# Kernel optimization log

Measured on AMD Instinct MI355X. Metric: run time of the kernel, lower is better.

The kernel has to match this reference:

```python
import jax, jax.numpy as jnp
import numpy as np

V, D, DC, L, K, H, ND, S, B = 16, 256, 128, 3, 16, 4, 3, 900, 16
HD = D // H
DMETA = 17           # [confidence(1) | layer_id(8) | iter(4) | pass(4)]
DSLOT = DC + DMETA
MAX_ITERS, MAX_PASSES, WRITE_TOK = 2, 2, 64
FLOATS = ['token_embed','segment_embed','slot_embeddings','layer_id_embeddings',
          'Wq_read','Wk_read','Wv_read','Wg_read','bg_read','Wqkv','Wo',
          'Wwk','Wwv','Wwg','bwg','Wout','bout','prev_answer_embed','Wfb','bfb']


def setup_inputs():
    key = jax.random.key(0)
    ks = jax.random.split(key, 24)
    n = lambda i, shape: 0.02 * jax.random.normal(ks[i], shape, dtype=jnp.float32)
    return dict(
        demo_inputs=jax.random.randint(ks[0], (B, ND, S), 0, V),
        demo_outputs=jax.random.randint(ks[1], (B, ND, S), 0, V),
        test_input=jax.random.randint(ks[2], (B, S), 0, V),
        token_embed=n(3, (V, D)), segment_embed=n(4, (2, D)),
        slot_embeddings=n(5, (L, K, DC)), layer_id_embeddings=n(6, (L, 8)),
        Wq_read=n(7, (L, D, DC)), Wk_read=n(8, (L, DSLOT, DC)), Wv_read=n(9, (L, DSLOT, D)),
        Wg_read=n(10, (L, D, 1)), bg_read=jnp.zeros((L, 1)),
        Wqkv=n(11, (L, D, 3 * D)), Wo=n(12, (L, D, D)),
        Wwk=n(13, (L, D, DC)), Wwv=n(14, (L, D, DC)),
        Wwg=n(15, (L, 2 * DC, 1)), bwg=jnp.zeros((L, 1)),
        Wout=n(16, (D, V)), bout=jnp.zeros((V,)),
        prev_answer_embed=n(17, (V, D)),
        Wfb=n(18, (2 * D, D)), bfb=jnp.zeros((D,)),
    )


def make_rope(n, hd):
    inv = 1.0 / (10000.0 ** (jnp.arange(0, hd, 2, dtype=jnp.float32) / hd))
    f = jnp.arange(n, dtype=jnp.float32)[:, None] * inv[None, :]  # [N, hd/2]
    return jnp.cos(f), jnp.sin(f)


def apply_rope(x, cos, sin):  # x: [B,H,N,hd]
    x1, x2 = x[..., ::2], x[..., 1::2]
    r1 = x1 * cos - x2 * sin
    r2 = x1 * sin + x2 * cos
    return jnp.stack([r1, r2], axis=-1).reshape(x.shape)


def layer_step(h, cache, l, it, pas, cos, sin, p):
    Bsz, N, _ = h.shape
    s0 = l * K
    # --- read: cross-attention from sequence to full structured cache ---
    q = h @ p['Wq_read'][l]                                   # [B,N,DC]
    k = cache @ p['Wk_read'][l]                               # [B,LK,DC]
    v = cache @ p['Wv_read'][l]                               # [B,LK,D]
    attn = jax.nn.softmax(jnp.einsum('bnd,bmd->bnm', q, k) / np.float32(np.sqrt(DC)), axis=-1)
    read = jnp.einsum('bnm,bmd->bnd', attn, v)
    rgate = jax.nn.sigmoid(h @ p['Wg_read'][l] + p['bg_read'][l])
    h = h + rgate * read
    # --- linear self-attention with RoPE (use_linear_attention=True) ---
    qh, kh, vh = jnp.split(h @ p['Wqkv'][l], 3, axis=-1)
    heads = lambda x: x.reshape(Bsz, N, H, HD).transpose(0, 2, 1, 3)
    qh, kh, vh = heads(qh), heads(kh), heads(vh)
    qf = jax.nn.elu(apply_rope(qh, cos, sin)) + 1.0
    kf = jax.nn.elu(apply_rope(kh, cos, sin)) + 1.0
    kv = jnp.einsum('bhnd,bhne->bhde', kf, vh)                # [B,H,HD,HD]
    z = 1.0 / (jnp.einsum('bhnd,bhd->bhn', qf, kf.sum(axis=2)) + 1e-6)
    att = jnp.einsum('bhnd,bhde->bhne', qf, kv) * z[..., None]
    h = h + att.transpose(0, 2, 1, 3).reshape(Bsz, N, D) @ p['Wo'][l]
    # --- write: last max_write_tokens tokens -> this layer's slot block ---
    wt = h[:, -WRITE_TOK:]                                    # [B,64,D]
    wk, wv = wt @ p['Wwk'][l], wt @ p['Wwv'][l]               # [B,64,DC]
    sq = cache[:, s0:s0 + K, :DC]                             # slot content queries
    wattn = jax.nn.softmax(jnp.einsum('bkd,bmd->bkm', sq, wk) / np.float32(np.sqrt(DC)), axis=-1)
    new_c = jnp.einsum('bkm,bmd->bkd', wattn, wv)
    wgate = jax.nn.sigmoid(jnp.concatenate([sq, new_c], -1) @ p['Wwg'][l] + p['bwg'][l])
    it_oh = jax.nn.one_hot(min(it, 3), 4, dtype=h.dtype)
    ps_oh = jax.nn.one_hot(min(pas, 3), 4, dtype=h.dtype)
    cache = cache.at[:, s0:s0 + K, :DC].set(sq + wgate * new_c)
    cache = cache.at[:, s0:s0 + K, DC:DC + 1].set(wgate)      # confidence
    cache = cache.at[:, s0:s0 + K, DC + 9:DC + 13].set(jnp.broadcast_to(it_oh, (Bsz, K, 4)))
    cache = cache.at[:, s0:s0 + K, DC + 13:].set(jnp.broadcast_to(ps_oh, (Bsz, K, 4)))
    return h, cache


def _model(p, demo_inputs, demo_outputs, test_input):
    Bsz = test_input.shape[0]
    # interleave demo_in/demo_out pairs then append test input
    demos = jnp.stack([demo_inputs, demo_outputs], axis=2).reshape(Bsz, ND * 2 * S)
    full = jnp.concatenate([demos, test_input], axis=1)       # [B, 6300]
    N = full.shape[1]
    cur = p['token_embed'][full] + p['segment_embed'][0]      # [B,N,D]
    cos, sin = make_rope(N, HD)
    # initial cache: learned content | conf=0 | layer_id | iter=0 | pass=0
    content = jnp.broadcast_to(p['slot_embeddings'].reshape(L * K, DC), (Bsz, L * K, DC))
    lids = jnp.broadcast_to(p['layer_id_embeddings'][:, None, :], (L, K, 8)).reshape(L * K, 8)
    meta = jnp.concatenate([jnp.zeros((L * K, 1)), lids, jnp.zeros((L * K, 8))], axis=-1)
    cache = jnp.concatenate([content, jnp.broadcast_to(meta, (Bsz, L * K, DMETA))], axis=-1)
    ts = ND * 2 * S
    prev_logits = None
    for pas in range(MAX_PASSES):
        if pas > 0:  # answer feedback from previous pass predictions
            pae = p['prev_answer_embed'][jnp.argmax(prev_logits, axis=-1)]
            tr = cur[:, ts:ts + S]
            g = jax.nn.sigmoid(jnp.concatenate([tr, pae], -1) @ p['Wfb'] + p['bfb'])
            cur = cur.at[:, ts:ts + S].set(tr + g * pae)
        h = cur
        for l in range(L):
            for it in range(MAX_ITERS):
                h, cache = layer_step(h, cache, l, it, pas, cos, sin, p)
        prev_logits = h[:, ts:ts + S] @ p['Wout'] + p['bout']  # [B,S,V]
    return prev_logits


def reference(demo_inputs, demo_outputs, test_input, token_embed, segment_embed,
              slot_embeddings, layer_id_embeddings, Wq_read, Wk_read, Wv_read,
              Wg_read, bg_read, Wqkv, Wo, Wwk, Wwv, Wwg, bwg, Wout, bout,
              prev_answer_embed, Wfb, bfb):
    p = dict(zip(FLOATS, (token_embed, segment_embed, slot_embeddings, layer_id_embeddings,
                          Wq_read, Wk_read, Wv_read, Wg_read, bg_read, Wqkv, Wo,
                          Wwk, Wwv, Wwg, bwg, Wout, bout, prev_answer_embed, Wfb, bfb)))
    return _model(p, demo_inputs, demo_outputs, test_input)
```

## Files before the change

kernel.cpp:

```cpp
#include <hip/hip_runtime.h>
#include <math.h>

#define Bz 16
#define Sz 900
#define Vz 16
#define Dz 256
#define DCz 128
#define Hz 4
#define Nz 6300
#define TSz 5400
#define DSLOTz 145
#define NSLOTz 48
#define GXA 99

typedef unsigned short u16;
typedef unsigned int u32;

typedef __bf16 bf16x8 __attribute__((ext_vector_type(8)));
typedef float floatx4 __attribute__((ext_vector_type(4)));
union U8 { bf16x8 v; uint4 q; };

static __device__ __forceinline__ float sigm(float x){ return 1.0f/(1.0f+__expf(-x)); }
static __device__ __forceinline__ void fma4(float4& a, float s, float4 b){ a.x+=s*b.x; a.y+=s*b.y; a.z+=s*b.z; a.w+=s*b.w; }
static __device__ __forceinline__ float dot4(float4 a, float4 b){ return a.x*b.x + a.y*b.y + a.z*b.z + a.w*b.w; }
static __device__ __forceinline__ float4 f4z(){ float4 z; z.x=0.f; z.y=0.f; z.z=0.f; z.w=0.f; return z; }
static __device__ __forceinline__ float elu1(float x){ return x>0.f ? x+1.f : __expf(x); }
static __device__ __forceinline__ float fcomp(float4 v, int i){ return (i==0)?v.x:(i==1)?v.y:(i==2)?v.z:v.w; }

static __device__ __forceinline__ uint hi16(float x){
  uint u = __float_as_uint(x);
  return (u + 0x7fffu + ((u>>16)&1u)) >> 16;
}

typedef const void GV __attribute__((address_space(1)));
typedef void LV __attribute__((address_space(3)));
static __device__ __forceinline__ void gl16(const float* g, float* l){
  __builtin_amdgcn_global_load_lds((GV*)g, (LV*)l, 16, 0, 0);
}
static __device__ __forceinline__ void gl16b(const void* g, void* l){
  __builtin_amdgcn_global_load_lds((GV*)g, (LV*)l, 16, 0, 0);
}

__global__ void k_sentinel(float* out, int nelem){
  int i = blockIdx.x*256 + threadIdx.x;
  if (i < nelem) out[i] = 12345.0f;
}

__global__ void k_zero(float* p, int n){
  int i = blockIdx.x*256 + threadIdx.x;
  if (i < n) p[i] = 0.f;
}

__global__ void k_rope(float* cost, float* sint){
  int i = blockIdx.x*256 + threadIdx.x;
  if (i >= Nz*32) return;
  int n = i>>5, f = i&31;
  double invd = pow(10000.0, -(double)f/32.0);
  double fr = (double)n * invd;
  cost[i] = (float)cos(fr);
  sint[i] = (float)sin(fr);
}

__global__ void k_embed(const int* __restrict__ di, const int* __restrict__ dq,
                        const int* __restrict__ ti, const float* __restrict__ temb,
                        const float* __restrict__ semb, float* __restrict__ h){
  int i = blockIdx.x*256 + threadIdx.x;
  if (i >= Bz*Nz*64) return;
  int dv = i & 63; int bn = i >> 6; int n = bn % Nz; int b = bn / Nz;
  int tok;
  if (n < TSz){
    int nd = n/1800; int r = n - nd*1800;
    tok = (r < Sz) ? di[(b*3+nd)*Sz + r] : dq[(b*3+nd)*Sz + (r-Sz)];
  } else {
    tok = ti[b*Sz + (n-TSz)];
  }
  const float4* e4 = (const float4*)(temb + (size_t)tok*Dz);
  const float4* s4 = (const float4*)semb;
  float4 v = e4[dv]; float4 s = s4[dv];
  v.x += s.x; v.y += s.y; v.z += s.z; v.w += s.w;
  ((float4*)h)[(size_t)bn*64 + dv] = v;
}

__global__ void k_cache_init(const float* __restrict__ slot_emb, const float* __restrict__ lid,
                             float* __restrict__ cache){
  int i = blockIdx.x*256 + threadIdx.x;
  if (i >= Bz*NSLOTz*DSLOTz) return;
  int c = i % DSLOTz; int sc = (i / DSLOTz) % NSLOTz; int l = sc >> 4;
  float v = 0.f;
  if (c < DCz) v = slot_emb[sc*DCz + c];
  else if (c >= 129 && c < 137) v = lid[l*8 + (c-129)];
  cache[i] = v;
}

__global__ void k_pack_w(const float* __restrict__ Wqkv,
                         u16* __restrict__ wh, u16* __restrict__ wl){
  int i = blockIdx.x*256 + threadIdx.x;
  if (i >= 3*65536) return;
  int l = i >> 16; int r = i & 65535;
  int ks = r >> 13; int ct = (r>>9)&15; int lane = (r>>3)&63; int e = r&7;
  int k = ks*32 + ((lane>>4)<<3) + e;
  int c = ct*16 + (lane&15);
  float x = Wqkv[(size_t)l*196608 + (size_t)k*768 + c];
  uint hb = hi16(x);
  uint lb = hi16(x - __uint_as_float(hb<<16));
  wh[i] = (u16)hb; wl[i] = (u16)lb;
}

__global__ void k_pack_wkv(const float* __restrict__ Wqkv,
                           u16* __restrict__ wh, u16* __restrict__ wl){
  int i = blockIdx.x*256 + threadIdx.x;
  if (i >= 3*131072) return;
  int l = i / 131072; int r = i % 131072;
  int ks = r >> 14; int ct = (r>>9)&31; int lane = (r>>3)&63; int e = r&7;
  int k = ks*32 + ((lane>>4)<<3) + e;
  int c = ct*16 + (lane&15);
  float x = Wqkv[(size_t)l*196608 + (size_t)k*768 + 256 + c];
  uint hb = hi16(x);
  uint lb = hi16(x - __uint_as_float(hb<<16));
  wh[i] = (u16)hb; wl[i] = (u16)lb;
}

__global__ void k_pack_wr(const float* __restrict__ Wqr,
                          u16* __restrict__ wh, u16* __restrict__ wl){
  int i = blockIdx.x*256 + threadIdx.x;
  if (i >= 3*32768) return;
  int l = i >> 15; int r = i & 32767;
  int ks = r >> 12; int ct = (r>>9)&7; int lane = (r>>3)&63; int e = r&7;
  int k = ks*32 + ((lane>>4)<<3) + e;
  int c = ct*16 + (lane&15);
  float x = Wqr[(size_t)l*32768 + (size_t)k*DCz + c];
  uint hb = hi16(x);
  uint lb = hi16(x - __uint_as_float(hb<<16));
  wh[i] = (u16)hb; wl[i] = (u16)lb;
}

__global__ void k_pack_p(const float* __restrict__ pmat,
                         u16* __restrict__ ph, u16* __restrict__ pl){
  int i = blockIdx.x*256 + threadIdx.x;
  if (i >= 16*65536) return;
  int b = i >> 16; int r = i & 65535;
  int ks2 = r >> 13; int ct = (r>>9)&15; int lane = (r>>3)&63; int e = r&7;
  int c = ks2*32 + ((lane>>4)<<3) + e;
  int oc = ct*16 + (lane&15);
  float x = pmat[(((size_t)(b*4 + (c>>6)))*64 + (c&63))*256 + oc];
  uint hb = hi16(x);
  uint lb = hi16(x - __uint_as_float(hb<<16));
  ph[i] = (u16)hb; pl[i] = (u16)lb;
}

__global__ __launch_bounds__(384) void k_proj_cache(const float* __restrict__ cache,
    const float* __restrict__ Wk, const float* __restrict__ Wv,
    u16* __restrict__ krh, u16* __restrict__ krl,
    u16* __restrict__ vrh, u16* __restrict__ vrl){
  __shared__ float crow[DSLOTz];
  int b = blockIdx.x / NSLOTz, sc = blockIdx.x % NSLOTz;
  int t = threadIdx.x;
  const float* cp = cache + (size_t)(b*NSLOTz+sc)*DSLOTz;
  if (t < DSLOTz) crow[t] = cp[t];
  __syncthreads();
  if (t < DCz){
    float a = 0.f;
    for (int r2=0;r2<DSLOTz;r2++) a += crow[r2]*Wk[r2*DCz + t];
    uint hb = hi16(a);
    uint lb = hi16(a - __uint_as_float(hb<<16));
    int ks = t>>5, st = sc>>4, lane = (sc&15) | (((t>>3)&3)<<4), e = t&7;
    size_t idx = (size_t)b*6144 + (size_t)(((ks*3+st)*64 + lane)*8 + e);
    krh[idx] = (u16)hb; krl[idx] = (u16)lb;
  } else {
    int d = t - DCz;
    float a = 0.f;
    for (int r2=0;r2<DSLOTz;r2++) a += crow[r2]*Wv[r2*Dz + d];
    uint hb = hi16(a);
    uint lb = hi16(a - __uint_as_float(hb<<16));
    int ot = d>>4, ks2 = sc>>5, lane = (d&15) | (((sc>>3)&3)<<4), e = sc&7;
    size_t idx = (size_t)b*16384 + (size_t)(((ks2*16+ot)*64 + lane)*8 + e);
    vrh[idx] = (u16)hb; vrl[idx] = (u16)lb;
  }
}

#define RA2_BH 0
#define RA2_BL 5120
#define RA2_QBH 10240
#define RA2_QBL 30720
#define RA2_ABH 10240
#define RA2_ABL 20480
#define RA2_G  51200
#define RA2_WG 51456
__global__ __launch_bounds__(256) void k_read_attn(
    float* __restrict__ h,
    const u16* __restrict__ wqh, const u16* __restrict__ wql,
    const u16* __restrict__ krh, const u16* __restrict__ krl,
    const u16* __restrict__ vrh, const u16* __restrict__ vrl,
    const float* __restrict__ Wg, const float* __restrict__ bg){
  __shared__ float smem[13120];
  char* sb = (char*)smem;
  const int t = threadIdx.x;
  const int b = blockIdx.y;
  const int n0 = blockIdx.x*64;
  const int w = t>>6, lane = t&63, ln = t&15, lq = (t>>4)&3;
  float* hb = h + (size_t)b*Nz*Dz;
  ((float*)(sb+RA2_WG))[t] = Wg[t];
  floatx4 acc[2][4];
  #pragma unroll
  for (int i=0;i<2;i++)
    #pragma unroll
    for (int j=0;j<4;j++){ acc[i][j][0]=0.f; acc[i][j][1]=0.f; acc[i][j][2]=0.f; acc[i][j][3]=0.f; }
  for (int ks=0; ks<8; ks++){
    __syncthreads();
    {
      int n = n0 + (t>>2);
      const float* hp = hb + (size_t)n*Dz + ks*32 + (t&3)*8;
      float x[8];
      if (n < Nz){
        float4 v0 = *(const float4*)(hp);
        float4 v1 = *(const float4*)(hp+4);
        x[0]=v0.x; x[1]=v0.y; x[2]=v0.z; x[3]=v0.w;
        x[4]=v1.x; x[5]=v1.y; x[6]=v1.z; x[7]=v1.w;
      } else {
        #pragma unroll
        for (int e=0;e<8;e++) x[e]=0.f;
      }
      uint hw[4], lw[4];
      #pragma unroll
      for (int e=0;e<4;e++){
        uint h0=hi16(x[2*e]), h1=hi16(x[2*e+1]);
        uint l0=hi16(x[2*e]-__uint_as_float(h0<<16));
        uint l1=hi16(x[2*e+1]-__uint_as_float(h1<<16));
        hw[e]=h0|(h1<<16); lw[e]=l0|(l1<<16);
      }
      int a16 = (((t>>2)*5 + (t&3))<<4);
      *(uint4*)(sb + RA2_BH + a16) = make_uint4(hw[0],hw[1],hw[2],hw[3]);
      *(uint4*)(sb + RA2_BL + a16) = make_uint4(lw[0],lw[1],lw[2],lw[3]);
    }
    __syncthreads();
    U8 bh[4], bl[4];
    #pragma unroll
    for (int nt=0; nt<4; nt++){
      int a16 = (((nt*16+ln)*5 + lq)<<4);
      bh[nt].q = *(const uint4*)(sb + RA2_BH + a16);
      bl[nt].q = *(const uint4*)(sb + RA2_BL + a16);
    }
    #pragma unroll
    for (int mf=0; mf<2; mf++){
      U8 ah, al;
      size_t ai = ((size_t)(ks*8 + w*2 + mf))*512 + lane*8;
      ah.q = *(const uint4*)(wqh + ai);
      al.q = *(const uint4*)(wql + ai);
      #pragma unroll
      for (int nt=0; nt<4; nt++){
        acc[mf][nt] = __builtin_amdgcn_mfma_f32_16x16x32_bf16(ah.v, bh[nt].v, acc[mf][nt], 0,0,0);
        acc[mf][nt] = __builtin_amdgcn_mfma_f32_16x16x32_bf16(ah.v, bl[nt].v, acc[mf][nt], 0,0,0);
        acc[mf][nt] = __builtin_amdgcn_mfma_f32_16x16x32_bf16(al.v, bh[nt].v, acc[mf][nt], 0,0,0);
      }
    }
  }
  {
    int n = t>>2, kq = t&3;
    int nn = n0+n; int nc = (nn < Nz) ? nn : (Nz-1);
    const float* hp = hb + (size_t)nc*Dz + kq*64;
    const float* wgp = (const float*)(sb+RA2_WG) + kq*64;
    float a = 0.f;
    for (int k=0;k<64;k+=4){
      float4 hv = *(const float4*)(hp+k);
      float4 wv = *(const float4*)(wgp+k);
      a += dot4(hv,wv);
    }
    a += __shfl_xor(a,1,64);
    a += __shfl_xor(a,2,64);
    if (kq==0) ((float*)(sb+RA2_G))[n] = a;
  }
  {
    #pragma unroll
    for (int mf=0; mf<2; mf++){
      #pragma unroll
      for (int nt=0; nt<4; nt++){
        float v0 = acc[mf][nt][0], v1 = acc[mf][nt][1];
        float v2 = acc[mf][nt][2], v3 = acc[mf][nt][3];
        uint h0=hi16(v0), h1=hi16(v1), h2=hi16(v2), h3=hi16(v3);
        uint l0=hi16(v0-__uint_as_float(h0<<16));
        uint l1=hi16(v1-__uint_as_float(h1<<16));
        uint l2=hi16(v2-__uint_as_float(h2<<16));
        uint l3=hi16(v3-__uint_as_float(h3<<16));
        int a16 = (((nt*16+ln)*5 + (mf*2 + (lq>>1)))<<4) + ((lq&1)<<3);
        *(uint2*)(sb + RA2_QBH + w*5120 + a16) = make_uint2(h0|(h1<<16), h2|(h3<<16));
        *(uint2*)(sb + RA2_QBL + w*5120 + a16) = make_uint2(l0|(l1<<16), l2|(l3<<16));
      }
    }
  }
  __syncthreads();
  floatx4 sacc[3];
  #pragma unroll
  for (int st=0; st<3; st++){ sacc[st][0]=0.f; sacc[st][1]=0.f; sacc[st][2]=0.f; sacc[st][3]=0.f; }
  for (int ks=0; ks<4; ks++){
    U8 bh, bl;
    int a16 = (((w*16+ln)*5 + lq)<<4);
    bh.q = *(const uint4*)(sb + RA2_QBH + ks*5120 + a16);
    bl.q = *(const uint4*)(sb + RA2_QBL + ks*5120 + a16);
    #pragma unroll
    for (int st=0; st<3; st++){
      U8 ah, al;
      size_t ai = (size_t)b*6144 + ((size_t)(ks*3+st))*512 + lane*8;
      ah.q = *(const uint4*)(krh + ai);
      al.q = *(const uint4*)(krl + ai);
      sacc[st] = __builtin_amdgcn_mfma_f32_16x16x32_bf16(ah.v, bh.v, sacc[st], 0,0,0);
      sacc[st] = __builtin_amdgcn_mfma_f32_16x16x32_bf16(ah.v, bl.v, sacc[st], 0,0,0);
      sacc[st] = __builtin_amdgcn_mfma_f32_16x16x32_bf16(al.v, bh.v, sacc[st], 0,0,0);
    }
  }
  {
    const float scl = 0.088388347648318447f;
    float mx = -1e30f;
    #pragma unroll
    for (int st=0; st<3; st++)
      #pragma unroll
      for (int r=0;r<4;r++){ sacc[st][r] *= scl; mx = fmaxf(mx, sacc[st][r]); }
    mx = fmaxf(mx, __shfl_xor(mx, 16, 64));
    mx = fmaxf(mx, __shfl_xor(mx, 32, 64));
    float su = 0.f;
    #pragma unroll
    for (int st=0; st<3; st++)
      #pragma unroll
      for (int r=0;r<4;r++){ float e = __expf(sacc[st][r]-mx); sacc[st][r]=e; su+=e; }
    su += __shfl_xor(su, 16, 64);
    su += __shfl_xor(su, 32, 64);
    float inv = 1.f/su;
    #pragma unroll
    for (int st=0; st<3; st++)
      #pragma unroll
      for (int r=0;r<4;r++) sacc[st][r] *= inv;
  }
  __syncthreads();
  {
    uint2 ah2[3], al2[3];
    #pragma unroll
    for (int st=0; st<3; st++){
      float v0=sacc[st][0], v1=sacc[st][1], v2=sacc[st][2], v3=sacc[st][3];
      uint h0=hi16(v0), h1=hi16(v1), h2=hi16(v2), h3=hi16(v3);
      uint l0=hi16(v0-__uint_as_float(h0<<16));
      uint l1=hi16(v1-__uint_as_float(h1<<16));
      uint l2=hi16(v2-__uint_as_float(h2<<16));
      uint l3=hi16(v3-__uint_as_float(h3<<16));
      ah2[st] = make_uint2(h0|(h1<<16), h2|(h3<<16));
      al2[st] = make_uint2(l0|(l1<<16), l2|(l3<<16));
    }
    int rb = (w*16+ln)*5;
    int sub = (lq&1)<<3;
    #pragma unroll
    for (int st=0; st<2; st++){
      int a16 = ((rb + st*2 + (lq>>1))<<4) + sub;
      *(uint2*)(sb + RA2_ABH + a16) = ah2[st];
      *(uint2*)(sb + RA2_ABL + a16) = al2[st];
    }
    {
      int a16 = ((rb + (lq>>1))<<4) + sub;
      *(uint2*)(sb + RA2_ABH + 5120 + a16) = ah2[2];
      *(uint2*)(sb + RA2_ABL + 5120 + a16) = al2[2];
      int z16 = ((rb + 2 + (lq>>1))<<4) + sub;
      *(uint2*)(sb + RA2_ABH + 5120 + z16) = make_uint2(0,0);
      *(uint2*)(sb + RA2_ABL + 5120 + z16) = make_uint2(0,0);
    }
  }
  __syncthreads();
  floatx4 o[4][4];
  #pragma unroll
  for (int i=0;i<4;i++)
    #pragma unroll
    for (int j=0;j<4;j++){ o[i][j][0]=0.f; o[i][j][1]=0.f; o[i][j][2]=0.f; o[i][j][3]=0.f; }
  #pragma unroll
  for (int ks2=0; ks2<2; ks2++){
    U8 bh[4], bl[4];
    #pragma unroll
    for (int nt=0; nt<4; nt++){
      int a16 = (((nt*16+ln)*5 + lq)<<4);
      bh[nt].q = *(const uint4*)(sb + RA2_ABH + ks2*5120 + a16);
      bl[nt].q = *(const uint4*)(sb + RA2_ABL + ks2*5120 + a16);
    }
    #pragma unroll
    for (int mf=0; mf<4; mf++){
      U8 ah, al;
      size_t ai = (size_t)b*16384 + ((size_t)(ks2*16 + w*4 + mf))*512 + lane*8;
      ah.q = *(const uint4*)(vrh + ai);
      al.q = *(const uint4*)(vrl + ai);
      #pragma unroll
      for (int nt=0; nt<4; nt++){
        o[mf][nt] = __builtin_amdgcn_mfma_f32_16x16x32_bf16(ah.v, bh[nt].v, o[mf][nt], 0,0,0);
        o[mf][nt] = __builtin_amdgcn_mfma_f32_16x16x32_bf16(ah.v, bl[nt].v, o[mf][nt], 0,0,0);
        o[mf][nt] = __builtin_amdgcn_mfma_f32_16x16x32_bf16(al.v, bh[nt].v, o[mf][nt], 0,0,0);
      }
    }
  }
  float bg0 = bg[0];
  #pragma unroll
  for (int nt=0; nt<4; nt++){
    int n = n0 + nt*16 + ln;
    if (n < Nz){
      float gv = sigm(((const float*)(sb+RA2_G))[nt*16+ln] + bg0);
      #pragma unroll
      for (int mf=0; mf<4; mf++){
        float* hp = hb + (size_t)n*Dz + w*64 + mf*16 + lq*4;
        float4 hv = *(const float4*)hp;
        hv.x += gv*o[mf][nt][0];
        hv.y += gv*o[mf][nt][1];
        hv.z += gv*o[mf][nt][2];
        hv.w += gv*o[mf][nt][3];
        *(float4*)hp = hv;
      }
    }
  }
}

#define KV_AH 0
#define KV_AL 16384
#define KV_BH 32768
#define KV_BL 37888
__global__ __launch_bounds__(256) void k_kv(
    const float* __restrict__ h,
    const u16* __restrict__ wh, const u16* __restrict__ wl,
    const float* __restrict__ cost, const float* __restrict__ sint,
    float* __restrict__ kvbuf){
  __shared__ float smem[10752];
  char* sb = (char*)smem;
  const int t = threadIdx.x;
  const int b = blockIdx.y;
  const int n0 = blockIdx.x*64;
  const int w = t>>6;
  const int lane = t&63;
  const int ln = t&15;
  const int lq = (t>>4)&3;
  const float* hb = h + (size_t)b*Nz*Dz;
  floatx4 acc[2][4][4];
  #pragma unroll
  for (int cp=0;cp<2;cp++)
    #pragma unroll
    for (int i=0;i<4;i++)
      #pragma unroll
      for (int j=0;j<4;j++){ acc[cp][i][j][0]=0.f; acc[cp][i][j][1]=0.f; acc[cp][i][j][2]=0.f; acc[cp][i][j][3]=0.f; }

  for (int ks=0; ks<8; ks++){
    __syncthreads();
    #pragma unroll
    for (int j=0;j<4;j++){
      int ct = w*4 + j;
      gl16b(wh + (((size_t)ks*32 + ct)<<9) + lane*8, sb + KV_AH + ct*1024);
      gl16b(wl + (((size_t)ks*32 + ct)<<9) + lane*8, sb + KV_AL + ct*1024);
    }
    {
      int n = n0 + (t>>2);
      const float* hp = hb + (size_t)n*Dz + ks*32 + (t&3)*8;
      float x[8];
      if (n < Nz){
        float4 v0 = *(const float4*)(hp);
        float4 v1 = *(const float4*)(hp+4);
        x[0]=v0.x; x[1]=v0.y; x[2]=v0.z; x[3]=v0.w;
        x[4]=v1.x; x[5]=v1.y; x[6]=v1.z; x[7]=v1.w;
      } else {
        #pragma unroll
        for (int e=0;e<8;e++) x[e]=0.f;
      }
      uint hw[4], lw[4];
      #pragma unroll
      for (int e=0;e<4;e++){
        uint h0=hi16(x[2*e]), h1=hi16(x[2*e+1]);
        uint l0=hi16(x[2*e]-__uint_as_float(h0<<16));
        uint l1=hi16(x[2*e+1]-__uint_as_float(h1<<16));
        hw[e]=h0|(h1<<16); lw[e]=l0|(l1<<16);
      }
      int a16 = (((t>>2)*5 + (t&3))<<4);
      *(uint4*)(sb + KV_BH + a16) = make_uint4(hw[0],hw[1],hw[2],hw[3]);
      *(uint4*)(sb + KV_BL + a16) = make_uint4(lw[0],lw[1],lw[2],lw[3]);
    }
    __syncthreads();
    U8 bh[4], bl[4];
    #pragma unroll
    for (int nt=0; nt<4; nt++){
      int a16 = (((nt*16+ln)*5 + lq)<<4);
      bh[nt].q = *(const uint4*)(sb + KV_BH + a16);
      bl[nt].q = *(const uint4*)(sb + KV_BL + a16);
    }
    #pragma unroll
    for (int mf=0; mf<4; mf++){
      U8 ah, al;
      int a16 = (((w*4+mf)*64 + lane)<<4);
      ah.q = *(const uint4*)(sb + KV_AH + a16);
      al.q = *(const uint4*)(sb + KV_AL + a16);
      #pragma unroll
      for (int nt=0; nt<4; nt++){
        acc[0][mf][nt] = __builtin_amdgcn_mfma_f32_16x16x32_bf16(ah.v, bh[nt].v, acc[0][mf][nt], 0,0,0);
        acc[0][mf][nt] = __builtin_amdgcn_mfma_f32_16x16x32_bf16(ah.v, bl[nt].v, acc[0][mf][nt], 0,0,0);
        acc[0][mf][nt] = __builtin_amdgcn_mfma_f32_16x16x32_bf16(al.v, bh[nt].v, acc[0][mf][nt], 0,0,0);
      }
    }
    __syncthreads();
    #pragma unroll
    for (int j=0;j<4;j++){
      int tl = w*4 + j;
      int ct = 16 + tl;
      gl16b(wh + (((size_t)ks*32 + ct)<<9) + lane*8, sb + KV_AH + tl*1024);
      gl16b(wl + (((size_t)ks*32 + ct)<<9) + lane*8, sb + KV_AL + tl*1024);
    }
    __syncthreads();
    #pragma unroll
    for (int mf=0; mf<4; mf++){
      U8 ah, al;
      int a16 = (((w*4+mf)*64 + lane)<<4);
      ah.q = *(const uint4*)(sb + KV_AH + a16);
      al.q = *(const uint4*)(sb + KV_AL + a16);
      #pragma unroll
      for (int nt=0; nt<4; nt++){
        acc[1][mf][nt] = __builtin_amdgcn_mfma_f32_16x16x32_bf16(ah.v, bh[nt].v, acc[1][mf][nt], 0,0,0);
        acc[1][mf][nt] = __builtin_amdgcn_mfma_f32_16x16x32_bf16(ah.v, bl[nt].v, acc[1][mf][nt], 0,0,0);
        acc[1][mf][nt] = __builtin_amdgcn_mfma_f32_16x16x32_bf16(al.v, bh[nt].v, acc[1][mf][nt], 0,0,0);
      }
    }
  }
  #pragma unroll
  for (int mf=0; mf<4; mf++){
    #pragma unroll
    for (int nt=0; nt<4; nt++){
      int n = n0 + nt*16 + ln;
      int valid = (n < Nz);
      int nc = valid ? n : (Nz-1);
      int pi = mf*8 + lq*2;
      float2 c2 = *(const float2*)(cost + (size_t)nc*32 + pi);
      float2 s2 = *(const float2*)(sint + (size_t)nc*32 + pi);
      float q0 = acc[0][mf][nt][0], q1 = acc[0][mf][nt][1];
      float q2 = acc[0][mf][nt][2], q3 = acc[0][mf][nt][3];
      float r0 = elu1(q0*c2.x - q1*s2.x);
      float r1 = elu1(q0*s2.x + q1*c2.x);
      float r2 = elu1(q2*c2.y - q3*s2.y);
      float r3 = elu1(q2*s2.y + q3*c2.y);
      acc[0][mf][nt][0] = valid ? r0 : 0.f;
      acc[0][mf][nt][1] = valid ? r1 : 0.f;
      acc[0][mf][nt][2] = valid ? r2 : 0.f;
      acc[0][mf][nt][3] = valid ? r3 : 0.f;
    }
  }
  const int d = t&63, q4 = t>>6;
  float* kvb = kvbuf + (size_t)(b*Hz)*4160;
  float* kfL = smem;
  float* vL  = smem + 4352;
  for (int g=0; g<4; g++){
    __syncthreads();
    if (w == g){
      #pragma unroll
      for (int mf=0; mf<4; mf++){
        #pragma unroll
        for (int nt=0; nt<4; nt++){
          int n = nt*16 + ln;
          int cc = mf*16 + lq*4;
          *(float4*)(kfL + n*68 + cc) = make_float4(acc[0][mf][nt][0],acc[0][mf][nt][1],acc[0][mf][nt][2],acc[0][mf][nt][3]);
          *(float4*)(vL  + n*68 + cc) = make_float4(acc[1][mf][nt][0],acc[1][mf][nt][1],acc[1][mf][nt][2],acc[1][mf][nt][3]);
        }
      }
    }
    __syncthreads();
    float4 kvacc[4];
    #pragma unroll
    for (int u=0;u<4;u++) kvacc[u]=f4z();
    float ksl = 0.f;
    for (int row=0; row<64; row++){
      float kd = kfL[row*68 + d];
      ksl += kd;
      const float4* vp = (const float4*)(vL + row*68);
      #pragma unroll
      for (int u=0;u<4;u++) fma4(kvacc[u], kd, vp[q4*4+u]);
    }
    float* kq = kvb + g*4160;
    #pragma unroll
    for (int u=0;u<4;u++){
      int e = q4*16 + 4*u;
      atomicAdd(&kq[(e+0)*64+d], kvacc[u].x);
      atomicAdd(&kq[(e+1)*64+d], kvacc[u].y);
      atomicAdd(&kq[(e+2)*64+d], kvacc[u].z);
      atomicAdd(&kq[(e+3)*64+d], kvacc[u].w);
    }
    if (q4==0) atomicAdd(&kq[4096+d], ksl);
  }
}

__global__ __launch_bounds__(256) void k_pmat(const float* __restrict__ kvbuf,
    const float* __restrict__ Wo, float* __restrict__ pmat){
  __shared__ float smem[8448];
  const int t = threadIdx.x;
  const int bh = blockIdx.x;
  const int hh = bh & 3;
  const int c0 = t&15, rr = t>>4;
  const float* kvp = kvbuf + (size_t)bh*4160;
  for (int id=t; id<4096; id+=256){
    int e=id>>6, d=id&63;
    smem[e*68+d] = kvp[id];
  }
  float4 acc[4][4];
  #pragma unroll
  for (int i=0;i<4;i++){
    #pragma unroll
    for (int j=0;j<4;j++) acc[i][j]=f4z();
  }
  for (int kt=0; kt<64; kt+=16){
    __syncthreads();
    for (int id=t; id<1024; id+=256){
      int wr=id>>6, cf=id&63;
      ((float4*)(smem+4352))[wr*64+cf] = ((const float4*)(Wo + (size_t)(hh*64+kt+wr)*256))[cf];
    }
    __syncthreads();
    for (int kk=0; kk<16; kk++){
      float4 a4 = *(const float4*)(smem + (kt+kk)*68 + 4*rr);
      const float4* wrow = (const float4*)(smem+4352) + kk*64;
      float4 w0=wrow[c0], w1=wrow[c0+16], w2=wrow[c0+32], w3=wrow[c0+48];
      #pragma unroll
      for (int i=0;i<4;i++){
        float ac = fcomp(a4,i);
        fma4(acc[i][0],ac,w0); fma4(acc[i][1],ac,w1); fma4(acc[i][2],ac,w2); fma4(acc[i][3],ac,w3);
      }
    }
  }
  float* Pp = pmat + (size_t)bh*16384;
  #pragma unroll
  for (int i=0;i<4;i++){
    #pragma unroll
    for (int j=0;j<4;j++) ((float4*)Pp)[(4*rr+i)*64 + c0 + 16*j] = acc[i][j];
  }
}

#define AH_OFF 0
#define AL_OFF 16384
#define BH_OFF 32768
#define BL_OFF 37888
#define KS_OFF 43008
__global__ __launch_bounds__(256) void k_att(
    float* __restrict__ h,
    const u16* __restrict__ wqh, const u16* __restrict__ wql,
    const u16* __restrict__ pth, const u16* __restrict__ ptl,
    const float* __restrict__ kvbuf,
    const float* __restrict__ cost, const float* __restrict__ sint){
  __shared__ float smem[11008];
  char* sb = (char*)smem;
  const int t = threadIdx.x;
  const int b = blockIdx.y;
  const int n0 = blockIdx.x*64;
  const int w = t>>6;
  const int lane = t&63;
  const int ln = t&15;
  const int lq = (t>>4)&3;
  float* hb = h + (size_t)b*Nz*Dz;
  ((float*)(sb+KS_OFF))[t] = kvbuf[(size_t)(b*Hz + w)*4160 + 4096 + lane];
  floatx4 acc[4][4];
  #pragma unroll
  for (int i=0;i<4;i++)
    #pragma unroll
    for (int j=0;j<4;j++){ acc[i][j][0]=0.f; acc[i][j][1]=0.f; acc[i][j][2]=0.f; acc[i][j][3]=0.f; }

  for (int ks=0; ks<8; ks++){
    __syncthreads();
    const u16* sh = wqh + (size_t)ks*8192;
    const u16* sl = wql + (size_t)ks*8192;
    #pragma unroll
    for (int j=0;j<4;j++){
      int c = w*4 + j;
      gl16b(sh + c*512 + lane*8, sb + AH_OFF + c*1024);
      gl16b(sl + c*512 + lane*8, sb + AL_OFF + c*1024);
    }
    {
      int n = n0 + (t>>2);
      const float* hp = hb + (size_t)n*Dz + ks*32 + (t&3)*8;
      float x[8];
      if (n < Nz){
        float4 v0 = *(const float4*)(hp);
        float4 v1 = *(const float4*)(hp+4);
        x[0]=v0.x; x[1]=v0.y; x[2]=v0.z; x[3]=v0.w;
        x[4]=v1.x; x[5]=v1.y; x[6]=v1.z; x[7]=v1.w;
      } else {
        #pragma unroll
        for (int e=0;e<8;e++) x[e]=0.f;
      }
      uint hw[4], lw[4];
      #pragma unroll
      for (int e=0;e<4;e++){
        uint h0=hi16(x[2*e]), h1=hi16(x[2*e+1]);
        uint l0=hi16(x[2*e]-__uint_as_float(h0<<16));
        uint l1=hi16(x[2*e+1]-__uint_as_float(h1<<16));
        hw[e]=h0|(h1<<16); lw[e]=l0|(l1<<16);
      }
      int a16 = (((t>>2)*5 + (t&3))<<4);
      *(uint4*)(sb + BH_OFF + a16) = make_uint4(hw[0],hw[1],hw[2],hw[3]);
      *(uint4*)(sb + BL_OFF + a16) = make_uint4(lw[0],lw[1],lw[2],lw[3]);
    }
    __syncthreads();
    U8 bh[4], bl[4];
    #pragma unroll
    for (int nt=0; nt<4; nt++){
      int a16 = (((nt*16+ln)*5 + lq)<<4);
      bh[nt].q = *(const uint4*)(sb + BH_OFF + a16);
      bl[nt].q = *(const uint4*)(sb + BL_OFF + a16);
    }
    #pragma unroll
    for (int mf=0; mf<4; mf++){
      U8 ah, al;
      int a16 = (((w*4+mf)*64 + lane)<<4);
      ah.q = *(const uint4*)(sb + AH_OFF + a16);
      al.q = *(const uint4*)(sb + AL_OFF + a16);
      #pragma unroll
      for (int nt=0; nt<4; nt++){
        acc[mf][nt] = __builtin_amdgcn_mfma_f32_16x16x32_bf16(ah.v, bh[nt].v, acc[mf][nt], 0,0,0);
        acc[mf][nt] = __builtin_amdgcn_mfma_f32_16x16x32_bf16(ah.v, bl[nt].v, acc[mf][nt], 0,0,0);
        acc[mf][nt] = __builtin_amdgcn_mfma_f32_16x16x32_bf16(al.v, bh[nt].v, acc[mf][nt], 0,0,0);
      }
    }
  }
  uint2 qzh[4][4], qzl[4][4];
  {
    float4 ks4[4];
    #pragma unroll
    for (int mf=0; mf<4; mf++)
      ks4[mf] = *(const float4*)(sb + KS_OFF + ((w*64 + mf*16 + lq*4)<<2));
    float psum[4] = {0.f,0.f,0.f,0.f};
    #pragma unroll
    for (int mf=0; mf<4; mf++){
      #pragma unroll
      for (int nt=0; nt<4; nt++){
        int n = n0 + nt*16 + ln;
        int nc = (n < Nz) ? n : (Nz-1);
        int pi = mf*8 + lq*2;
        float2 c2 = *(const float2*)(cost + (size_t)nc*32 + pi);
        float2 s2 = *(const float2*)(sint + (size_t)nc*32 + pi);
        float q0 = acc[mf][nt][0], q1 = acc[mf][nt][1];
        float q2 = acc[mf][nt][2], q3 = acc[mf][nt][3];
        float r0 = elu1(q0*c2.x - q1*s2.x);
        float r1 = elu1(q0*s2.x + q1*c2.x);
        float r2 = elu1(q2*c2.y - q3*s2.y);
        float r3 = elu1(q2*s2.y + q3*c2.y);
        acc[mf][nt][0]=r0; acc[mf][nt][1]=r1; acc[mf][nt][2]=r2; acc[mf][nt][3]=r3;
        psum[nt] += r0*ks4[mf].x + r1*ks4[mf].y + r2*ks4[mf].z + r3*ks4[mf].w;
      }
    }
    float zt[4];
    #pragma unroll
    for (int nt=0; nt<4; nt++){
      float p = psum[nt];
      p += __shfl_xor(p, 16, 64);
      p += __shfl_xor(p, 32, 64);
      zt[nt] = 1.f/(p + 1e-6f);
    }
    #pragma unroll
    for (int mf=0; mf<4; mf++){
      #pragma unroll
      for (int nt=0; nt<4; nt++){
        float v0 = acc[mf][nt][0]*zt[nt];
        float v1 = acc[mf][nt][1]*zt[nt];
        float v2 = acc[mf][nt][2]*zt[nt];
        float v3 = acc[mf][nt][3]*zt[nt];
        uint h0=hi16(v0), h1=hi16(v1), h2=hi16(v2), h3=hi16(v3);
        qzh[mf][nt] = make_uint2(h0|(h1<<16), h2|(h3<<16));
        uint l0=hi16(v0-__uint_as_float(h0<<16));
        uint l1=hi16(v1-__uint_as_float(h1<<16));
        uint l2=hi16(v2-__uint_as_float(h2<<16));
        uint l3=hi16(v3-__uint_as_float(h3<<16));
        qzl[mf][nt] = make_uint2(l0|(l1<<16), l2|(l3<<16));
      }
    }
  }
  floatx4 acc2[4][4];
  #pragma unroll
  for (int i=0;i<4;i++)
    #pragma unroll
    for (int j=0;j<4;j++){ acc2[i][j][0]=0.f; acc2[i][j][1]=0.f; acc2[i][j][2]=0.f; acc2[i][j][3]=0.f; }
  for (int ks2=0; ks2<8; ks2++){
    __syncthreads();
    const u16* sh = pth + (size_t)(b*8 + ks2)*8192;
    const u16* sl = ptl + (size_t)(b*8 + ks2)*8192;
    #pragma unroll
    for (int j=0;j<4;j++){
      int c = w*4 + j;
      gl16b(sh + c*512 + lane*8, sb + AH_OFF + c*1024);
      gl16b(sl + c*512 + lane*8, sb + AL_OFF + c*1024);
    }
    if (w == (ks2>>1)){
      #pragma unroll
      for (int mm=0; mm<2; mm++){
        int mf = ((ks2&1)<<1) + mm;
        int g = (mm<<1) + (lq>>1);
        int sub = (lq&1)*8;
        #pragma unroll
        for (int nt=0; nt<4; nt++){
          int a16 = (((nt*16+ln)*5 + g)<<4) + sub;
          *(uint2*)(sb + BH_OFF + a16) = qzh[mf][nt];
          *(uint2*)(sb + BL_OFF + a16) = qzl[mf][nt];
        }
      }
    }
    __syncthreads();
    U8 bh[4], bl[4];
    #pragma unroll
    for (int nt=0; nt<4; nt++){
      int a16 = (((nt*16+ln)*5 + lq)<<4);
      bh[nt].q = *(const uint4*)(sb + BH_OFF + a16);
      bl[nt].q = *(const uint4*)(sb + BL_OFF + a16);
    }
    #pragma unroll
    for (int mf=0; mf<4; mf++){
      U8 ah, al;
      int a16 = (((w*4+mf)*64 + lane)<<4);
      ah.q = *(const uint4*)(sb + AH_OFF + a16);
      al.q = *(const uint4*)(sb + AL_OFF + a16);
      #pragma unroll
      for (int nt=0; nt<4; nt++){
        acc2[mf][nt] = __builtin_amdgcn_mfma_f32_16x16x32_bf16(ah.v, bh[nt].v, acc2[mf][nt], 0,0,0);
        acc2[mf][nt] = __builtin_amdgcn_mfma_f32_16x16x32_bf16(ah.v, bl[nt].v, acc2[mf][nt], 0,0,0);
        acc2[mf][nt] = __builtin_amdgcn_mfma_f32_16x16x32_bf16(al.v, bh[nt].v, acc2[mf][nt], 0,0,0);
      }
    }
  }
  #pragma unroll
  for (int mf=0; mf<4; mf++){
    #pragma unroll
    for (int nt=0; nt<4; nt++){
      int n = n0 + nt*16 + ln;
      if (n < Nz){
        float* hp = hb + (size_t)n*Dz + w*64 + mf*16 + lq*4;
        float4 hv = *(const float4*)hp;
        hv.x += acc2[mf][nt][0];
        hv.y += acc2[mf][nt][1];
        hv.z += acc2[mf][nt][2];
        hv.w += acc2[mf][nt][3];
        *(float4*)hp = hv;
      }
    }
  }
}

__global__ __launch_bounds__(256) void k_wkv(const float* __restrict__ h,
    const float* __restrict__ Wwk, const float* __restrict__ Wwv,
    float* __restrict__ wkbuf, float* __restrict__ wvbuf){
  __shared__ float wtL[16*257];
  int t = threadIdx.x;
  int b = blockIdx.y, m0 = blockIdx.x*16;
  const float* hb = h + ((size_t)b*Nz + (Nz-64))*Dz;
  for (int i=t;i<16*Dz;i+=256){ int r=i>>8,c=i&255; wtL[r*257+c] = hb[(size_t)(m0+r)*Dz + c]; }
  __syncthreads();
  int r=t>>4, c0=t&15;
  float4 ak0=f4z(),ak1=f4z(),av0=f4z(),av1=f4z();
  for (int kk=0;kk<Dz;kk++){
    float hv = wtL[r*257+kk];
    const float4* wk4 = (const float4*)(Wwk + (size_t)kk*DCz);
    const float4* wv4 = (const float4*)(Wwv + (size_t)kk*DCz);
    fma4(ak0,hv,wk4[c0]); fma4(ak1,hv,wk4[c0+16]);
    fma4(av0,hv,wv4[c0]); fma4(av1,hv,wv4[c0+16]);
  }
  float4* ok = (float4*)(wkbuf + (size_t)(b*64 + m0+r)*DCz);
  float4* ov = (float4*)(wvbuf + (size_t)(b*64 + m0+r)*DCz);
  ok[c0]=ak0; ok[c0+16]=ak1; ov[c0]=av0; ov[c0+16]=av1;
}

__global__ __launch_bounds__(256) void k_cache_upd(float* __restrict__ cache,
    const float* __restrict__ wkbuf, const float* __restrict__ wvbuf,
    const float* __restrict__ Wwg, const float* __restrict__ bwg,
    int s0, int it, int pas){
  __shared__ float sqL[16*132];
  __shared__ float wkL[64*132];
  __shared__ float wat[16*68];
  __shared__ float ncL[16*132];
  __shared__ float wg[16];
  int t = threadIdx.x; int b = blockIdx.x;
  for (int i=t;i<16*DCz;i+=256){ int k2=i>>7,c=i&127; sqL[k2*132+c] = cache[((size_t)(b*NSLOTz)+s0+k2)*DSLOTz + c]; }
  for (int i=t;i<64*DCz;i+=256){ int m=i>>7,c=i&127; wkL[m*132+c] = wkbuf[(size_t)(b*64+m)*DCz+c]; }
  __syncthreads();
  {
    int k2 = t>>4;
    const float4* s4 = (const float4*)(sqL) + k2*33;
    for (int mm=0;mm<4;mm++){
      int m = (t&15) + 16*mm;
      const float4* k4 = (const float4*)(wkL) + m*33;
      float a=0.f;
      for (int d4=0;d4<32;d4++) a += dot4(s4[d4], k4[d4]);
      wat[k2*68+m] = a * 0.088388347648318447f;
    }
  }
  __syncthreads();
  if (t<16){
    float mx=-1e30f;
    for (int m=0;m<64;m++) mx = fmaxf(mx, wat[t*68+m]);
    float su=0.f;
    for (int m=0;m<64;m++){ float e=__expf(wat[t*68+m]-mx); wat[t*68+m]=e; su+=e; }
    float inv=1.f/su;
    for (int m=0;m<64;m++) wat[t*68+m]*=inv;
  }
  __syncthreads();
  {
    int k2=t>>4, c0=t&15;
    float4 a0=f4z(), a1=f4z();
    const float4* wvg = (const float4*)(wvbuf + (size_t)b*64*DCz);
    for (int m=0;m<64;m++){
      float a = wat[k2*68+m];
      fma4(a0,a,wvg[m*32+c0]); fma4(a1,a,wvg[m*32+c0+16]);
    }
    ((float4*)ncL)[k2*33+c0]=a0; ((float4*)ncL)[k2*33+16+c0]=a1;
  }
  __syncthreads();
  if (t<16){
    float a = bwg[0];
    for (int d2=0; d2<DCz; d2++) a += sqL[t*132+d2]*Wwg[d2] + ncL[t*132+d2]*Wwg[DCz+d2];
    wg[t] = sigm(a);
  }
  __syncthreads();
  for (int i=t;i<16*DCz;i+=256){
    int k2=i>>7,c=i&127;
    cache[((size_t)(b*NSLOTz)+s0+k2)*DSLOTz + c] = sqL[k2*132+c] + wg[k2]*ncL[k2*132+c];
  }
  if (t<16){
    float* cp = cache + ((size_t)(b*NSLOTz)+s0+t)*DSLOTz;
    cp[128] = wg[t];
    cp[137] = (it==0)?1.f:0.f; cp[138] = (it==1)?1.f:0.f; cp[139]=0.f; cp[140]=0.f;
    cp[141] = (pas==0)?1.f:0.f; cp[142] = (pas==1)?1.f:0.f; cp[143]=0.f; cp[144]=0.f;
  }
}

__global__ __launch_bounds__(256) void k_logits(const float* __restrict__ h,
    const float* __restrict__ Wout, const float* __restrict__ bout, float* __restrict__ out){
  __shared__ float hl[16*257];
  int t = threadIdx.x; int row0 = blockIdx.x*16;
  for (int i=t;i<16*Dz;i+=256){
    int rr=i>>8,c=i&255; int row=row0+rr; int b=row/Sz, s=row-b*Sz;
    hl[rr*257+c] = h[((size_t)b*Nz + TSz + s)*Dz + c];
  }
  __syncthreads();
  int rr = t>>4, v = t&15;
  float a = bout[v];
  for (int c=0;c<Dz;c++) a += hl[rr*257+c]*Wout[c*Vz + v];
  out[(size_t)(row0+rr)*Vz + v] = a;
}

__global__ __launch_bounds__(256) void k_feedback(float* __restrict__ h,
    const float* __restrict__ logits0, const float* __restrict__ pae,
    const float* __restrict__ Wfb, const float* __restrict__ bfb){
  __shared__ float trL[16*257];
  __shared__ float paeL[16*257];
  __shared__ int amL[16];
  int t = threadIdx.x; int b = blockIdx.y; int s0 = blockIdx.x*16;
  if (t<16){
    int s = s0+t; int am=0;
    if (s < Sz){
      const float* lg = logits0 + (size_t)(b*Sz+s)*Vz;
      float best = lg[0];
      for (int v=1;v<16;v++){ if (lg[v] > best){ best=lg[v]; am=v; } }
    }
    amL[t]=am;
  }
  for (int i=t;i<16*Dz;i+=256){
    int rr=i>>8,c=i&255; int s=s0+rr;
    trL[rr*257+c] = (s<Sz)? h[((size_t)b*Nz + TSz + s)*Dz + c] : 0.f;
  }
  __syncthreads();
  for (int i=t;i<16*Dz;i+=256){ int rr=i>>8,c=i&255; paeL[rr*257+c] = pae[(size_t)amL[rr]*Dz + c]; }
  __syncthreads();
  int r=t>>4, c0=t&15;
  float4 acc[4]; acc[0]=f4z(); acc[1]=f4z(); acc[2]=f4z(); acc[3]=f4z();
  for (int kk=0;kk<Dz;kk++){
    float xv = trL[r*257+kk];
    const float4* wr = (const float4*)(Wfb + (size_t)kk*Dz);
    fma4(acc[0],xv,wr[c0]); fma4(acc[1],xv,wr[c0+16]); fma4(acc[2],xv,wr[c0+32]); fma4(acc[3],xv,wr[c0+48]);
  }
  for (int kk=0;kk<Dz;kk++){
    float xv = paeL[r*257+kk];
    const float4* wr = (const float4*)(Wfb + (size_t)(Dz+kk)*Dz);
    fma4(acc[0],xv,wr[c0]); fma4(acc[1],xv,wr[c0+16]); fma4(acc[2],xv,wr[c0+32]); fma4(acc[3],xv,wr[c0+48]);
  }
  int s = s0+r;
  if (s < Sz){
    float* cp = h + ((size_t)b*Nz + TSz + s)*Dz;
    #pragma unroll
    for (int j=0;j<4;j++){
      float vals[4] = {acc[j].x, acc[j].y, acc[j].z, acc[j].w};
      #pragma unroll
      for (int q2=0;q2<4;q2++){
        int c = (c0+16*j)*4 + q2;
        float g = sigm(vals[q2] + bfb[c]);
        cp[c] = trL[r*257+c] + g*paeL[r*257+c];
      }
    }
  }
}

extern "C" void kernel_launch(void* const* d_in, const int* in_sizes, int n_in,
                              void* d_out, int out_size, void* d_ws, size_t ws_size,
                              hipStream_t stream){
  (void)in_sizes; (void)n_in;
  const int*   demo_in   = (const int*)d_in[0];
  const int*   demo_out  = (const int*)d_in[1];
  const int*   test_in   = (const int*)d_in[2];
  const float* token_emb = (const float*)d_in[3];
  const float* seg_emb   = (const float*)d_in[4];
  const float* slot_emb  = (const float*)d_in[5];
  const float* lid_emb   = (const float*)d_in[6];
  const float* Wq_read   = (const float*)d_in[7];
  const float* Wk_read   = (const float*)d_in[8];
  const float* Wv_read   = (const float*)d_in[9];
  const float* Wg_read   = (const float*)d_in[10];
  const float* bg_read   = (const float*)d_in[11];
  const float* Wqkv      = (const float*)d_in[12];
  const float* Wo        = (const float*)d_in[13];
  const float* Wwk       = (const float*)d_in[14];
  const float* Wwv       = (const float*)d_in[15];
  const float* Wwg       = (const float*)d_in[16];
  const float* bwg       = (const float*)d_in[17];
  const float* Wout      = (const float*)d_in[18];
  const float* bout      = (const float*)d_in[19];
  const float* pae       = (const float*)d_in[20];
  const float* Wfb       = (const float*)d_in[21];
  const float* bfb       = (const float*)d_in[22];

  char* wsb = (char*)d_ws;
  size_t off = 0;
  auto alloc = [&](size_t bytes)->char*{
    char* p = wsb + off;
    off += (bytes + 255) & ~(size_t)255;
    return p;
  };
  float* hbuf   = (float*)alloc((size_t)Bz*Nz*Dz*4);
  float* cache  = (float*)alloc((size_t)Bz*NSLOTz*DSLOTz*4);
  float* kvbuf  = (float*)alloc((size_t)Bz*Hz*4160*4);
  float* pmat   = (float*)alloc((size_t)Bz*Hz*64*256*4);
  float* wkbuf  = (float*)alloc((size_t)Bz*64*DCz*4);
  float* wvbuf  = (float*)alloc((size_t)Bz*64*DCz*4);
  float* logits0= (float*)alloc((size_t)Bz*Sz*Vz*4);
  float* cost   = (float*)alloc((size_t)Nz*32*4);
  float* sint   = (float*)alloc((size_t)Nz*32*4);
  u16*   wqth   = (u16*)alloc((size_t)3*65536*2);
  u16*   wqtl   = (u16*)alloc((size_t)3*65536*2);
  u16*   pth    = (u16*)alloc((size_t)16*65536*2);
  u16*   ptl    = (u16*)alloc((size_t)16*65536*2);
  u16*   wkvh   = (u16*)alloc((size_t)3*131072*2);
  u16*   wkvl   = (u16*)alloc((size_t)3*131072*2);
  u16*   wqrh   = (u16*)alloc((size_t)3*32768*2);
  u16*   wqrl   = (u16*)alloc((size_t)3*32768*2);
  u16*   krh    = (u16*)alloc((size_t)Bz*6144*2);
  u16*   krl    = (u16*)alloc((size_t)Bz*6144*2);
  u16*   vrh    = (u16*)alloc((size_t)Bz*16384*2);
  u16*   vrl    = (u16*)alloc((size_t)Bz*16384*2);

  if (off > ws_size){
    k_sentinel<<<(out_size+255)/256, 256, 0, stream>>>((float*)d_out, out_size);
    return;
  }

  k_rope<<<(Nz*32+255)/256, 256, 0, stream>>>(cost, sint);
  k_cache_init<<<(Bz*NSLOTz*DSLOTz+255)/256, 256, 0, stream>>>(slot_emb, lid_emb, cache);
  k_pack_w<<<768, 256, 0, stream>>>(Wqkv, wqth, wqtl);
  k_pack_wkv<<<1536, 256, 0, stream>>>(Wqkv, wkvh, wkvl);
  k_pack_wr<<<384, 256, 0, stream>>>(Wq_read, wqrh, wqrl);
  k_zero<<<512, 256, 0, stream>>>((float*)vrh, Bz*16384/2);
  k_zero<<<512, 256, 0, stream>>>((float*)vrl, Bz*16384/2);

  const int KVN = Bz*Hz*4160;
  for (int pas=0; pas<2; pas++){
    k_embed<<<(Bz*Nz*64+255)/256, 256, 0, stream>>>(demo_in, demo_out, test_in, token_emb, seg_emb, hbuf);
    if (pas==1)
      k_feedback<<<dim3(57,Bz), 256, 0, stream>>>(hbuf, logits0, pae, Wfb, bfb);
    for (int l=0; l<3; l++){
      for (int it=0; it<2; it++){
        k_proj_cache<<<Bz*NSLOTz, 384, 0, stream>>>(cache,
            Wk_read + (size_t)l*DSLOTz*DCz, Wv_read + (size_t)l*DSLOTz*Dz,
            krh, krl, vrh, vrl);
        k_read_attn<<<dim3(GXA,Bz), 256, 0, stream>>>(hbuf,
            wqrh + (size_t)l*32768, wqrl + (size_t)l*32768,
            krh, krl, vrh, vrl,
            Wg_read + (size_t)l*Dz, bg_read + l);
        k_zero<<<(KVN+255)/256, 256, 0, stream>>>(kvbuf, KVN);
        k_kv<<<dim3(GXA,Bz), 256, 0, stream>>>(hbuf,
            wkvh + (size_t)l*131072, wkvl + (size_t)l*131072, cost, sint, kvbuf);
        k_pmat<<<Bz*Hz, 256, 0, stream>>>(kvbuf, Wo + (size_t)l*Dz*Dz, pmat);
        k_pack_p<<<4096, 256, 0, stream>>>(pmat, pth, ptl);
        k_att<<<dim3(GXA,Bz), 256, 0, stream>>>(hbuf,
            wqth + (size_t)l*65536, wqtl + (size_t)l*65536, pth, ptl,
            kvbuf, cost, sint);
        k_wkv<<<dim3(4,Bz), 256, 0, stream>>>(hbuf,
            Wwk + (size_t)l*Dz*DCz, Wwv + (size_t)l*Dz*DCz, wkbuf, wvbuf);
        k_cache_upd<<<Bz, 256, 0, stream>>>(cache, wkbuf, wvbuf,
            Wwg + (size_t)l*2*DCz, bwg + l, l*16, it, pas);
      }
    }
    float* outp = (pas==0) ? logits0 : (float*)d_out;
    k_logits<<<900, 256, 0, stream>>>(hbuf, Wout, bout, outp);
  }
}
```

Measured before the change: 8.263 ms.

## Replace k_kv atomics with per-block partials and load weights directly from global

k_kv now reads the packed Wkv fragments straight from global memory into registers instead of staging them through shared memory, which removes several barriers per k-step and shrinks LDS use. When workspace allows, each block writes its KV partial sums to a dedicated buffer instead of using atomicAdd, and k_pmat reduces the 99 partials serially. The zeroing kernel is skipped in that mode. The cost is a large extra workspace buffer and a serial 99-way reduction inside only 64 k_pmat blocks, which could become a bottleneck.

New measurement: 9.425 ms. 1.14x slower.

```diff
diff --git a/kernel.cpp b/kernel.cpp
--- a/kernel.cpp
+++ b/kernel.cpp
@@ -409,16 +409,14 @@
   }
 }
 
-#define KV_AH 0
-#define KV_AL 16384
-#define KV_BH 32768
-#define KV_BL 37888
+#define KV_BH 0
+#define KV_BL 5120
 __global__ __launch_bounds__(256) void k_kv(
     const float* __restrict__ h,
     const u16* __restrict__ wh, const u16* __restrict__ wl,
     const float* __restrict__ cost, const float* __restrict__ sint,
-    float* __restrict__ kvbuf){
-  __shared__ float smem[10752];
+    float* __restrict__ kvpart, float* __restrict__ kvbuf, int use_part){
+  __shared__ float smem[8704];
   char* sb = (char*)smem;
   const int t = threadIdx.x;
   const int b = blockIdx.y;
@@ -438,12 +436,6 @@
 
   for (int ks=0; ks<8; ks++){
     __syncthreads();
-    #pragma unroll
-    for (int j=0;j<4;j++){
-      int ct = w*4 + j;
-      gl16b(wh + (((size_t)ks*32 + ct)<<9) + lane*8, sb + KV_AH + ct*1024);
-      gl16b(wl + (((size_t)ks*32 + ct)<<9) + lane*8, sb + KV_AL + ct*1024);
-    }
     {
       int n = n0 + (t>>2);
       const float* hp = hb + (size_t)n*Dz + ks*32 + (t&3)*8;
@@ -478,38 +470,19 @@
       bl[nt].q = *(const uint4*)(sb + KV_BL + a16);
     }
     #pragma unroll
-    for (int mf=0; mf<4; mf++){
-      U8 ah, al;
-      int a16 = (((w*4+mf)*64 + lane)<<4);
-      ah.q = *(const uint4*)(sb + KV_AH + a16);
-      al.q = *(const uint4*)(sb + KV_AL + a16);
-      #pragma unroll
-      for (int nt=0; nt<4; nt++){
-        acc[0][mf][nt] = __builtin_amdgcn_mfma_f32_16x16x32_bf16(ah.v, bh[nt].v, acc[0][mf][nt], 0,0,0);
-        acc[0][mf][nt] = __builtin_amdgcn_mfma_f32_16x16x32_bf16(ah.v, bl[nt].v, acc[0][mf][nt], 0,0,0);
-        acc[0][mf][nt] = __builtin_amdgcn_mfma_f32_16x16x32_bf16(al.v, bh[nt].v, acc[0][mf][nt], 0,0,0);
-      }
-    }
-    __syncthreads();
-    #pragma unroll
-    for (int j=0;j<4;j++){
-      int tl = w*4 + j;
-      int ct = 16 + tl;
-      gl16b(wh + (((size_t)ks*32 + ct)<<9) + lane*8, sb + KV_AH + tl*1024);
-      gl16b(wl + (((size_t)ks*32 + ct)<<9) + lane*8, sb + KV_AL + tl*1024);
-    }
-    __syncthreads();
-    #pragma unroll
-    for (int mf=0; mf<4; mf++){
-      U8 ah, al;
-      int a16 = (((w*4+mf)*64 + lane)<<4);
-      ah.q = *(const uint4*)(sb + KV_AH + a16);
-      al.q = *(const uint4*)(sb + KV_AL + a16);
-      #pragma unroll
-      for (int nt=0; nt<4; nt++){
-        acc[1][mf][nt] = __builtin_amdgcn_mfma_f32_16x16x32_bf16(ah.v, bh[nt].v, acc[1][mf][nt], 0,0,0);
-        acc[1][mf][nt] = __builtin_amdgcn_mfma_f32_16x16x32_bf16(ah.v, bl[nt].v, acc[1][mf][nt], 0,0,0);
-        acc[1][mf][nt] = __builtin_amdgcn_mfma_f32_16x16x32_bf16(al.v, bh[nt].v, acc[1][mf][nt], 0,0,0);
+    for (int cp=0; cp<2; cp++){
+      #pragma unroll
+      for (int mf=0; mf<4; mf++){
+        U8 ah, al;
+        size_t ai = ((size_t)(ks*32 + cp*16 + w*4 + mf))*512 + lane*8;
+        ah.q = *(const uint4*)(wh + ai);
+        al.q = *(const uint4*)(wl + ai);
+        #pragma unroll
+        for (int nt=0; nt<4; nt++){
+          acc[cp][mf][nt] = __builtin_amdgcn_mfma_f32_16x16x32_bf16(ah.v, bh[nt].v, acc[cp][mf][nt], 0,0,0);
+          acc[cp][mf][nt] = __builtin_amdgcn_mfma_f32_16x16x32_bf16(ah.v, bl[nt].v, acc[cp][mf][nt], 0,0,0);
+          acc[cp][mf][nt] = __builtin_amdgcn_mfma_f32_16x16x32_bf16(al.v, bh[nt].v, acc[cp][mf][nt], 0,0,0);
+        }
       }
     }
   }
@@ -536,7 +509,6 @@
     }
   }
   const int d = t&63, q4 = t>>6;
-  float* kvb = kvbuf + (size_t)(b*Hz)*4160;
   float* kfL = smem;
   float* vL  = smem + 4352;
   for (int g=0; g<4; g++){
@@ -565,30 +537,54 @@
       #pragma unroll
       for (int u=0;u<4;u++) fma4(kvacc[u], kd, vp[q4*4+u]);
     }
-    float* kq = kvb + g*4160;
-    #pragma unroll
-    for (int u=0;u<4;u++){
-      int e = q4*16 + 4*u;
-      atomicAdd(&kq[(e+0)*64+d], kvacc[u].x);
-      atomicAdd(&kq[(e+1)*64+d], kvacc[u].y);
-      atomicAdd(&kq[(e+2)*64+d], kvacc[u].z);
-      atomicAdd(&kq[(e+3)*64+d], kvacc[u].w);
-    }
-    if (q4==0) atomicAdd(&kq[4096+d], ksl);
-  }
-}
-
-__global__ __launch_bounds__(256) void k_pmat(const float* __restrict__ kvbuf,
-    const float* __restrict__ Wo, float* __restrict__ pmat){
+    if (use_part){
+      float* kq = kvpart + ((size_t)((b*Hz + g)*GXA) + blockIdx.x)*4160;
+      #pragma unroll
+      for (int u=0;u<4;u++){
+        int e = q4*16 + 4*u;
+        kq[(e+0)*64+d] = kvacc[u].x;
+        kq[(e+1)*64+d] = kvacc[u].y;
+        kq[(e+2)*64+d] = kvacc[u].z;
+        kq[(e+3)*64+d] = kvacc[u].w;
+      }
+      if (q4==0) kq[4096+d] = ksl;
+    } else {
+      float* kq = kvbuf + ((size_t)(b*Hz + g))*4160;
+      #pragma unroll
+      for (int u=0;u<4;u++){
+        int e = q4*16 + 4*u;
+        atomicAdd(&kq[(e+0)*64+d], kvacc[u].x);
+        atomicAdd(&kq[(e+1)*64+d], kvacc[u].y);
+        atomicAdd(&kq[(e+2)*64+d], kvacc[u].z);
+        atomicAdd(&kq[(e+3)*64+d], kvacc[u].w);
+      }
+      if (q4==0) atomicAdd(&kq[4096+d], ksl);
+    }
+  }
+}
+
+__global__ __launch_bounds__(256) void k_pmat(
+    const float* __restrict__ kvpart, float* __restrict__ kvbuf,
+    const float* __restrict__ Wo, float* __restrict__ pmat, int use_part){
   __shared__ float smem[8448];
   const int t = threadIdx.x;
   const int bh = blockIdx.x;
   const int hh = bh & 3;
   const int c0 = t&15, rr = t>>4;
-  const float* kvp = kvbuf + (size_t)bh*4160;
-  for (int id=t; id<4096; id+=256){
-    int e=id>>6, d=id&63;
-    smem[e*68+d] = kvp[id];
+  if (use_part){
+    const float* pp = kvpart + (size_t)bh*GXA*4160;
+    for (int id=t; id<4160; id+=256){
+      float a = 0.f;
+      for (int bx=0; bx<GXA; bx++) a += pp[(size_t)bx*4160 + id];
+      if (id < 4096) smem[(id>>6)*68 + (id&63)] = a;
+      else kvbuf[(size_t)bh*4160 + id] = a;
+    }
+  } else {
+    const float* kvp = kvbuf + (size_t)bh*4160;
+    for (int id=t; id<4096; id+=256){
+      int e=id>>6, d=id&63;
+      smem[e*68+d] = kvp[id];
+    }
   }
   float4 acc[4][4];
   #pragma unroll
@@ -1037,10 +1033,14 @@
   u16*   vrh    = (u16*)alloc((size_t)Bz*16384*2);
   u16*   vrl    = (u16*)alloc((size_t)Bz*16384*2);
 
-  if (off > ws_size){
+  size_t off_base = off;
+  if (off_base > ws_size){
     k_sentinel<<<(out_size+255)/256, 256, 0, stream>>>((float*)d_out, out_size);
     return;
   }
+  float* kvpart = (float*)alloc((size_t)Bz*Hz*GXA*4160*4);
+  int use_part = (off <= ws_size) ? 1 : 0;
+  if (!use_part){ off = off_base; kvpart = kvbuf;  }
 
   k_rope<<<(Nz*32+255)/256, 256, 0, stream>>>(cost, sint);
   k_cache_init<<<(Bz*NSLOTz*DSLOTz+255)/256, 256, 0, stream>>>(slot_emb, lid_emb, cache);
@@ -1064,10 +1064,12 @@
             wqrh + (size_t)l*32768, wqrl + (size_t)l*32768,
             krh, krl, vrh, vrl,
             Wg_read + (size_t)l*Dz, bg_read + l);
-        k_zero<<<(KVN+255)/256, 256, 0, stream>>>(kvbuf, KVN);
+        if (!use_part)
+          k_zero<<<(KVN+255)/256, 256, 0, stream>>>(kvbuf, KVN);
         k_kv<<<dim3(GXA,Bz), 256, 0, stream>>>(hbuf,
-            wkvh + (size_t)l*131072, wkvl + (size_t)l*131072, cost, sint, kvbuf);
-        k_pmat<<<Bz*Hz, 256, 0, stream>>>(kvbuf, Wo + (size_t)l*Dz*Dz, pmat);
+            wkvh + (size_t)l*131072, wkvl + (size_t)l*131072, cost, sint,
+            kvpart, kvbuf, use_part);
+        k_pmat<<<Bz*Hz, 256, 0, stream>>>(kvpart, kvbuf, Wo + (size_t)l*Dz*Dz, pmat, use_part);
         k_pack_p<<<4096, 256, 0, stream>>>(pmat, pth, ptl);
         k_att<<<dim3(GXA,Bz), 256, 0, stream>>>(hbuf,
             wqth + (size_t)l*65536, wqtl + (size_t)l*65536, pth, ptl,
```
